# Kernel optimization log

Measured on AMD Instinct MI355X. Metric: run time of the kernel, lower is better.

Reference implementation:

```python
import jax, jax.numpy as jnp
import numpy as np

OBS, SEQ = 8, 12          # observed steps, predicted steps (seq_len init arg)
G, P = 96, 16             # scenes x pedestrians per scene (uniform groups)
B = G * P                 # 1536
H, E, BOT, MID = 128, 64, 1024, 512


def setup_inputs() -> dict:
    key = jax.random.key(0)
    ks = jax.random.split(key, 26)
    rn = lambda k, sh, s=0.05: jax.random.normal(k, sh, jnp.float32) * s
    starts = jnp.arange(G, dtype=jnp.int64) * P
    return {
        "obs_traj": rn(ks[0], (OBS, B, 2), 1.0),
        "obs_traj_rel": rn(ks[1], (OBS, B, 2), 1.0),
        "typeID_seq": rn(ks[2], (OBS, B, 1), 1.0),
        "h0": rn(ks[3], (1, B, H), 0.1),
        "c0": rn(ks[4], (1, B, H), 0.1),
        "seq_start_end": jnp.stack([starts, starts + P], axis=1),
        # decoder spatial embedding Linear(2, E)
        "W_emb": rn(ks[5], (E, 2)), "b_emb": rn(ks[6], (E,)),
        # LSTM(E, H) weights, gate order i,f,g,o (PyTorch convention)
        "W_ih": rn(ks[7], (4 * H, E)), "b_ih": rn(ks[8], (4 * H,)),
        "W_hh": rn(ks[9], (4 * H, H)), "b_hh": rn(ks[10], (4 * H,)),
        # hidden2pos Linear(H, 2)
        "W_pos": rn(ks[11], (2, H)), "b_pos": rn(ks[12], (2,)),
        # PoolHiddenNet: spatial_embedding Linear(2, E), mlp_pre_pool [E+H, 512, BOT]
        "Wp_emb": rn(ks[13], (E, 2)), "bp_emb": rn(ks[14], (E,)),
        "Wp1": rn(ks[15], (MID, E + H)), "bp1": rn(ks[16], (MID,)),
        "Wp2": rn(ks[17], (BOT, MID)), "bp2": rn(ks[18], (BOT,)),
        # Decoder mlp [H+BOT, mlp_dim, H]
        "Wm1": rn(ks[19], (1024, H + BOT)), "bm1": rn(ks[20], (1024,)),
        "Wm2": rn(ks[21], (H, 1024)), "bm2": rn(ks[22], (H,)),
    }


def _forward(obs_traj, obs_traj_rel, h0, c0,
             W_emb, b_emb, W_ih, b_ih, W_hh, b_hh, W_pos, b_pos,
             Wp_emb, bp_emb, Wp1, bp1, Wp2, bp2, Wm1, bm1, Wm2, bm2):
    batch = obs_traj.shape[1]

    def pool(h, pos):
        # uniform groups: h_states.view(-1,H)[start:end] == reshape to (G,P,H)
        hh = h.reshape(G, P, H)
        pp = pos.reshape(G, P, 2)
        # torch semantics: row (i,j) holds pos[j]-pos[i] and hidden[j]
        rel = pp[:, None, :, :] - pp[:, :, None, :]          # (G,Pi,Pj,2)
        emb = rel @ Wp_emb.T + bp_emb                        # (G,Pi,Pj,E)
        hb = jnp.broadcast_to(hh[:, None, :, :], (G, P, P, H))
        x = jnp.concatenate([emb, hb], axis=-1)              # (G,Pi,Pj,E+H)
        x = jax.nn.relu(x @ Wp1.T + bp1)
        x = jax.nn.relu(x @ Wp2.T + bp2)                     # (G,Pi,Pj,BOT)
        return x.max(axis=2).reshape(batch, BOT)             # max over neighbors j

    def step(carry, _):
        h, c, last_pos, dec_in = carry
        gates = dec_in @ W_ih.T + b_ih + h @ W_hh.T + b_hh
        i, f, g, o = jnp.split(gates, 4, axis=-1)
        c = jax.nn.sigmoid(f) * c + jax.nn.sigmoid(i) * jnp.tanh(g)
        h = jax.nn.sigmoid(o) * jnp.tanh(c)
        rel_pos = h @ W_pos.T + b_pos                        # (B,2)
        curr_pos = rel_pos + last_pos
        pool_h = pool(h, curr_pos)
        ctx = jnp.concatenate([h, pool_h], axis=-1)          # (B,H+BOT)
        h = jax.nn.relu(jax.nn.relu(ctx @ Wm1.T + bm1) @ Wm2.T + bm2)
        dec_in = rel_pos @ W_emb.T + b_emb
        return (h, c, curr_pos, dec_in), rel_pos

    dec_in0 = obs_traj_rel[-1] @ W_emb.T + b_emb
    carry0 = (h0[0], c0[0], obs_traj[-1], dec_in0)
    (h, c, _, _), rels = jax.lax.scan(step, carry0, None, length=SEQ)
    return rels, h[None]                                     # (SEQ,B,2), (1,B,H)


def reference(obs_traj, obs_traj_rel, typeID_seq, h0, c0, seq_start_end,
              W_emb, b_emb, W_ih, b_ih, W_hh, b_hh, W_pos, b_pos,
              Wp_emb, bp_emb, Wp1, bp1, Wp2, bp2, Wm1, bm1, Wm2, bm2):
    # typeID_seq / seq_start_end unused math-wise (typeID module off; groups uniform)
    return _forward(obs_traj, obs_traj_rel, h0, c0,
                    W_emb, b_emb, W_ih, b_ih, W_hh, b_hh, W_pos, b_pos,
                    Wp_emb, bp_emb, Wp1, bp1, Wp2, bp2, Wm1, bm1, Wm2, bm2)
```

## Files before the change

### kernel.cpp

```cpp
#include <hip/hip_runtime.h>
#include <math.h>

#define OBS 8
#define SEQL 12
#define G 96
#define PP 16
#define B 1536
#define HD 128
#define ED 64
#define BOT 1024
#define MIDD 512
#define CTXD (HD + BOT)
#define MLPH 1024

typedef __attribute__((ext_vector_type(8))) short bf16x8;
typedef __attribute__((ext_vector_type(4))) float f32x4;

__device__ inline short f2bf(float x) {
    union { float f; unsigned u; } v; v.f = x;
    unsigned r = v.u + 0x7fffu + ((v.u >> 16) & 1u);
    return (short)(r >> 16);
}

__global__ void swizzleB_kernel(const float* __restrict__ src, unsigned short* __restrict__ dst,
                                int NT, int K, int total) {
    int u = blockIdx.x * 256 + threadIdx.x;
    if (u >= total) return;
    int l = u & 63; int v = u >> 6; int nt = v % NT; int kt = v / NT;
    int n = nt * 16 + (l & 15);
    int k = kt * 32 + ((l >> 4) << 3);
    const float* s = src + n * K + k;
    float4 s0 = *(const float4*)s;
    float4 s1 = *(const float4*)(s + 4);
    bf16x8 o;
    o[0] = f2bf(s0.x); o[1] = f2bf(s0.y); o[2] = f2bf(s0.z); o[3] = f2bf(s0.w);
    o[4] = f2bf(s1.x); o[5] = f2bf(s1.y); o[6] = f2bf(s1.z); o[7] = f2bf(s1.w);
    *(bf16x8*)(dst + u * 8) = o;
}

__global__ void swizzle_cat_kernel(const float* __restrict__ W_ih, const float* __restrict__ W_hh,
                                   unsigned short* __restrict__ dst) {
    int u = blockIdx.x * 256 + threadIdx.x;
    if (u >= 6 * 32 * 64) return;
    int l = u & 63; int v = u >> 6; int nt = v & 31; int kt = v >> 5;
    int n = nt * 16 + (l & 15);
    int k0 = kt * 32 + ((l >> 4) << 3);
    bf16x8 o;
#pragma unroll
    for (int e = 0; e < 8; ++e) {
        int k = k0 + e;
        float val = (k < ED) ? W_ih[n * ED + k] : W_hh[n * HD + (k - ED)];
        o[e] = f2bf(val);
    }
    *(bf16x8*)(dst + u * 8) = o;
}

__global__ void swizzle_p1_kernel(const float* __restrict__ Wp1,
                                  const float* __restrict__ CV,
                                  unsigned short* __restrict__ dst) {
    int u = blockIdx.x * 256 + threadIdx.x;
    if (u >= 5 * 32 * 64) return;
    int l = u & 63; int v = u >> 6; int nt = v & 31; int kt = v >> 5;
    int n = nt * 16 + (l & 15);
    int k0 = kt * 32 + ((l >> 4) << 3);
    bf16x8 o;
#pragma unroll
    for (int e = 0; e < 8; ++e) {
        int k = k0 + e;
        float val;
        if (k < HD)           val = Wp1[n * (ED + HD) + ED + k];
        else if (k == HD + 2) val = CV[n];
        else                  val = 0.f;
        o[e] = f2bf(val);
    }
    *(bf16x8*)(dst + u * 8) = o;
}

__global__ void mcvec_kernel(const float* __restrict__ Wp1, const float* __restrict__ Wp_emb,
                             const float* __restrict__ bp_emb, const float* __restrict__ bp1,
                             float* __restrict__ M0, float* __restrict__ M1, float* __restrict__ CV) {
    int r = blockIdx.x * blockDim.x + threadIdx.x;
    if (r >= MIDD) return;
    float m0 = 0.f, m1 = 0.f, cv = 0.f;
    for (int e = 0; e < ED; ++e) {
        float w = Wp1[r * (ED + HD) + e];
        m0 += w * Wp_emb[e * 2 + 0];
        m1 += w * Wp_emb[e * 2 + 1];
        cv += w * bp_emb[e];
    }
    M0[r] = m0; M1[r] = m1; CV[r] = cv + bp1[r];
}

__global__ void m01f_kernel(const float* __restrict__ M0, const float* __restrict__ M1,
                            float* __restrict__ M0F, float* __restrict__ M1F) {
    int id = blockIdx.x * 256 + threadIdx.x;
    if (id >= 16 * 64 * 8) return;
    int e = id & 7;
    int lane = (id >> 3) & 63;
    int kt = id >> 9;
    int k = kt * 32 + ((lane >> 4) << 3) + e;
    M0F[id] = M0[k];
    M1F[id] = M1[k];
}

__global__ void init_kernel(const float* __restrict__ obs_traj, const float* __restrict__ obs_traj_rel,
                            const float* __restrict__ h0, const float* __restrict__ c0,
                            const float* __restrict__ W_emb, const float* __restrict__ b_emb,
                            float* __restrict__ Hb, float* __restrict__ Cb,
                            float* __restrict__ POSb, float* __restrict__ DIN) {
    int b = blockIdx.x;
    int t = threadIdx.x;
    Hb[b * HD + t] = h0[b * HD + t];
    Cb[b * HD + t] = c0[b * HD + t];
    if (t < 2) POSb[b * 2 + t] = obs_traj[((OBS - 1) * B + b) * 2 + t];
    if (t < ED) {
        float rx = obs_traj_rel[((OBS - 1) * B + b) * 2 + 0];
        float ry = obs_traj_rel[((OBS - 1) * B + b) * 2 + 1];
        DIN[b * ED + t] = W_emb[t * 2 + 0] * rx + W_emb[t * 2 + 1] * ry + b_emb[t];
    }
}

__global__ __launch_bounds__(512) void step_kernel(
    const unsigned short* __restrict__ WcatF, const float* __restrict__ b_ih,
    const float* __restrict__ b_hh,
    const float* __restrict__ W_pos, const float* __restrict__ b_pos,
    const float* __restrict__ W_emb, const float* __restrict__ b_emb,
    const unsigned short* __restrict__ Wp1F2,
    float* __restrict__ Hb, float* __restrict__ Cb, float* __restrict__ POSb,
    float* __restrict__ DIN, unsigned short* __restrict__ Hbf,
    float* __restrict__ AbF, float* __restrict__ rel_out) {

    __shared__ unsigned short gf[6 * 64 * 8];
    __shared__ unsigned short a2f[5 * 64 * 8];
    __shared__ float hsh[16 * HD];
    __shared__ float relsh[16][4];

    int gsc = blockIdx.x;
    int t = threadIdx.x;
    int lane = t & 63, w = t >> 6;
    int colid = lane & 15, quad = lane >> 4;

    if (t < 384) {
        int kt = t >> 6;
        int j = lane & 15;
        int b = gsc * PP + j;
        int k0 = kt * 32 + ((lane >> 4) << 3);
        float4 x0, x1;
        if (k0 < ED) {
            const float4* p = (const float4*)(DIN + b * ED + k0);
            x0 = p[0]; x1 = p[1];
        } else {
            const float4* p = (const float4*)(Hb + b * HD + (k0 - ED));
            x0 = p[0]; x1 = p[1];
        }
        bf16x8 o;
        o[0] = f2bf(x0.x); o[1] = f2bf(x0.y); o[2] = f2bf(x0.z); o[3] = f2bf(x0.w);
        o[4] = f2bf(x1.x); o[5] = f2bf(x1.y); o[6] = f2bf(x1.z); o[7] = f2bf(x1.w);
        *(bf16x8*)(gf + t * 8) = o;
    }
    __syncthreads();

    f32x4 acc[4];
#pragma unroll
    for (int gi = 0; gi < 4; ++gi) acc[gi] = (f32x4)0.f;
#pragma unroll
    for (int kt = 0; kt < 6; ++kt) {
        bf16x8 af = *(const bf16x8*)(gf + (kt * 64 + lane) * 8);
#pragma unroll
        for (int gi = 0; gi < 4; ++gi) {
            bf16x8 bfr = *(const bf16x8*)(WcatF + ((kt * 32 + gi * 8 + w) * 64 + lane) * 8);
            acc[gi] = __builtin_amdgcn_mfma_f32_16x16x32_bf16(af, bfr, acc[gi], 0, 0, 0);
        }
    }
    int hcol = w * 16 + colid;
    float bias[4];
#pragma unroll
    for (int gi = 0; gi < 4; ++gi) {
        int n = (gi * 8 + w) * 16 + colid;
        bias[gi] = b_ih[n] + b_hh[n];
    }
#pragma unroll
    for (int r = 0; r < 4; ++r) {
        int row = quad * 4 + r;
        int b = gsc * PP + row;
        float gI = acc[0][r] + bias[0];
        float gF = acc[1][r] + bias[1];
        float gG = acc[2][r] + bias[2];
        float gO = acc[3][r] + bias[3];
        float c = Cb[b * HD + hcol];
        float cn = (1.f / (1.f + expf(-gF))) * c + (1.f / (1.f + expf(-gI))) * tanhf(gG);
        float hn = (1.f / (1.f + expf(-gO))) * tanhf(cn);
        Cb[b * HD + hcol] = cn;
        Hbf[b * HD + hcol] = (unsigned short)f2bf(hn);
        hsh[row * HD + hcol] = hn;
    }
    __syncthreads();

    {
        int row = t >> 5, kk = t & 31;
        float r0 = 0.f, r1 = 0.f;
#pragma unroll
        for (int q = 0; q < 4; ++q) {
            int k = kk + q * 32;
            float hv = hsh[row * HD + k];
            r0 = fmaf(hv, W_pos[k], r0);
            r1 = fmaf(hv, W_pos[HD + k], r1);
        }
#pragma unroll
        for (int m = 16; m >= 1; m >>= 1) {
            r0 += __shfl_xor(r0, m, 64);
            r1 += __shfl_xor(r1, m, 64);
        }
        if (kk == 0) {
            int b = gsc * PP + row;
            r0 += b_pos[0]; r1 += b_pos[1];
            float px = POSb[b * 2 + 0] + r0;
            float py = POSb[b * 2 + 1] + r1;
            POSb[b * 2 + 0] = px; POSb[b * 2 + 1] = py;
            rel_out[b * 2 + 0] = r0; rel_out[b * 2 + 1] = r1;
            relsh[row][0] = r0; relsh[row][1] = r1; relsh[row][2] = px; relsh[row][3] = py;
        }
    }
    __syncthreads();

#pragma unroll
    for (int rep = 0; rep < 2; ++rep) {
        int idx = rep * 512 + t;
        int row = idx >> 6, e = idx & 63;
        int b = gsc * PP + row;
        DIN[b * ED + e] = W_emb[e * 2 + 0] * relsh[row][0] +
                          W_emb[e * 2 + 1] * relsh[row][1] + b_emb[e];
    }
    if (t < 320) {
        int kt = t >> 6;
        int j = lane & 15;
        int k0 = kt * 32 + ((lane >> 4) << 3);
        bf16x8 o;
#pragma unroll
        for (int e = 0; e < 8; ++e) {
            int k = k0 + e;
            float v;
            if (k < HD)            v = hsh[j * HD + k];
            else if (k == HD + 2)  v = 1.f;
            else                   v = 0.f;
            o[e] = f2bf(v);
        }
        *(bf16x8*)(a2f + t * 8) = o;
    }
    __syncthreads();

    f32x4 acc2[4];
#pragma unroll
    for (int q = 0; q < 4; ++q) acc2[q] = (f32x4)0.f;
#pragma unroll
    for (int kt = 0; kt < 5; ++kt) {
        bf16x8 af = *(const bf16x8*)(a2f + (kt * 64 + lane) * 8);
#pragma unroll
        for (int q = 0; q < 4; ++q) {
            bf16x8 bfr = *(const bf16x8*)(Wp1F2 + ((kt * 32 + w * 4 + q) * 64 + lane) * 8);
            acc2[q] = __builtin_amdgcn_mfma_f32_16x16x32_bf16(af, bfr, acc2[q], 0, 0, 0);
        }
    }
#pragma unroll
    for (int q = 0; q < 4; ++q)
#pragma unroll
        for (int r = 0; r < 4; ++r) {
            int j = quad * 4 + r;
            int k = (w * 4 + q) * 16 + colid;
            int kt2 = k >> 5, lk = (k >> 3) & 3, e = k & 7;
            AbF[((gsc * 16 + kt2) * 64 + lk * 16 + j) * 8 + e] = acc2[q][r];
        }
}

__global__ __launch_bounds__(256, 3) void pool_gemm9_kernel(
    const float* __restrict__ AbF, const float* __restrict__ POSb,
    const float* __restrict__ M0F, const float* __restrict__ M1F,
    const unsigned short* __restrict__ Wp2F, const float* __restrict__ bp2,
    unsigned short* __restrict__ POOLbf) {

    __shared__ __align__(16) unsigned short Bst[2][8 * 64 * 8];
    __shared__ __align__(16) float Ust[2][64 * 8];
    __shared__ __align__(16) float M0st[2][64 * 8];
    __shared__ __align__(16) float M1st[2][64 * 8];

    int bi = blockIdx.x;
    int g = bi % 96;
    int rest = bi / 96;
    int io = rest >> 3;
    int colq = rest & 7;
    int t = threadIdx.x, lane = t & 63, w = t >> 6;
    int i0 = io * 8 + w * 2;
    int j = lane & 15;
    int ntb = colq * 8;

    float pjx = POSb[(g * PP + j) * 2 + 0];
    float pjy = POSb[(g * PP + j) * 2 + 1];
    float dx[2], dy[2];
#pragma unroll
    for (int p = 0; p < 2; ++p) {
        int gi = g * PP + i0 + p;
        dx[p] = pjx - POSb[gi * 2 + 0];
        dy[p] = pjy - POSb[gi * 2 + 1];
    }

    const float* ag = AbF + (size_t)g * (16 * 64 * 8);

    auto stage = [&](int kt, int buf) {
#pragma unroll
        for (int r = 0; r < 2; ++r) {
            int u = r * 256 + t;
            int nt = u >> 6, l = u & 63;
            *(bf16x8*)&Bst[buf][u * 8] =
                *(const bf16x8*)(Wp2F + ((kt * 64 + ntb + nt) * 64 + l) * 8);
        }
        if (t < 128) {
            *(float4*)&Ust[buf][t * 4] = *(const float4*)(ag + kt * 512 + t * 4);
            *(float4*)&M1st[buf][t * 4] = *(const float4*)(M1F + kt * 512 + t * 4);
        } else {
            int q = t - 128;
            *(float4*)&M0st[buf][q * 4] = *(const float4*)(M0F + kt * 512 + q * 4);
        }
    };

    f32x4 acc[2][8];
#pragma unroll
    for (int p = 0; p < 2; ++p)
#pragma unroll
        for (int n = 0; n < 8; ++n) acc[p][n] = (f32x4)0.f;

    stage(0, 0);
    __syncthreads();

    for (int kt = 0; kt < 16; ++kt) {
        int buf = kt & 1;
        if (kt < 15) stage(kt + 1, buf ^ 1);

        const float4* up = (const float4*)&Ust[buf][lane * 8];
        float4 u0 = up[0], u1 = up[1];
        const float4* m0p = (const float4*)&M0st[buf][lane * 8];
        float4 m00 = m0p[0], m01 = m0p[1];
        const float4* m1p = (const float4*)&M1st[buf][lane * 8];
        float4 m10 = m1p[0], m11 = m1p[1];

        bf16x8 af[2];
#pragma unroll
        for (int p = 0; p < 2; ++p) {
            float dxp = dx[p], dyp = dy[p];
            af[p][0] = f2bf(fmaxf(fmaf(m10.x, dyp, fmaf(m00.x, dxp, u0.x)), 0.f));
            af[p][1] = f2bf(fmaxf(fmaf(m10.y, dyp, fmaf(m00.y, dxp, u0.y)), 0.f));
            af[p][2] = f2bf(fmaxf(fmaf(m10.z, dyp, fmaf(m00.z, dxp, u0.z)), 0.f));
            af[p][3] = f2bf(fmaxf(fmaf(m10.w, dyp, fmaf(m00.w, dxp, u0.w)), 0.f));
            af[p][4] = f2bf(fmaxf(fmaf(m11.x, dyp, fmaf(m01.x, dxp, u1.x)), 0.f));
            af[p][5] = f2bf(fmaxf(fmaf(m11.y, dyp, fmaf(m01.y, dxp, u1.y)), 0.f));
            af[p][6] = f2bf(fmaxf(fmaf(m11.z, dyp, fmaf(m01.z, dxp, u1.z)), 0.f));
            af[p][7] = f2bf(fmaxf(fmaf(m11.w, dyp, fmaf(m01.w, dxp, u1.w)), 0.f));
        }
#pragma unroll
        for (int ng = 0; ng < 2; ++ng) {
            bf16x8 bfr[4];
#pragma unroll
            for (int n = 0; n < 4; ++n)
                bfr[n] = *(const bf16x8*)&Bst[buf][((ng * 4 + n) * 64 + lane) * 8];
#pragma unroll
            for (int n = 0; n < 4; ++n) {
                acc[0][ng * 4 + n] =
                    __builtin_amdgcn_mfma_f32_16x16x32_bf16(af[0], bfr[n], acc[0][ng * 4 + n], 0, 0, 0);
                acc[1][ng * 4 + n] =
                    __builtin_amdgcn_mfma_f32_16x16x32_bf16(af[1], bfr[n], acc[1][ng * 4 + n], 0, 0, 0);
            }
        }
        __syncthreads();
    }

    int quad = lane >> 4, colid = lane & 15;
#pragma unroll
    for (int p = 0; p < 2; ++p) {
        int i = g * PP + i0 + p;
#pragma unroll
        for (int n = 0; n < 8; ++n) {
            float m = fmaxf(fmaxf(acc[p][n][0], acc[p][n][1]),
                            fmaxf(acc[p][n][2], acc[p][n][3]));
            m = fmaxf(m, __shfl_xor(m, 16, 64));
            m = fmaxf(m, __shfl_xor(m, 32, 64));
            if (quad == 0) {
                int col = (ntb + n) * 16 + colid;
                float v = fmaxf(m + bp2[col], 0.f);
                POOLbf[i * BOT + col] = (unsigned short)f2bf(v);
            }
        }
    }
}

__global__ __launch_bounds__(256) void mlp1_mfma_kernel(
    const unsigned short* __restrict__ Hbf, const unsigned short* __restrict__ POOLbf,
    const unsigned short* __restrict__ Wm1F, const float* __restrict__ bm1,
    unsigned short* __restrict__ Y1Mbf) {

    __shared__ unsigned short a_f[16 * 64 * 8];
    int mg = blockIdx.x;
    int ng = blockIdx.y;
    int t = threadIdx.x, lane = t & 63, w = t >> 6;
    int rh = w >> 1, nh = w & 1;

    f32x4 acc[2][2];
#pragma unroll
    for (int a = 0; a < 2; ++a)
#pragma unroll
        for (int b = 0; b < 2; ++b) acc[a][b] = (f32x4)0.f;

    for (int c = 0; c < 9; ++c) {
        __syncthreads();
#pragma unroll
        for (int u0 = 0; u0 < 1024; u0 += 256) {
            int u = u0 + t;
            int rg = u >> 8, kt = (u >> 6) & 3, l = u & 63;
            int row = mg * 64 + rg * 16 + (l & 15);
            int kl = kt * 32 + ((l >> 4) << 3);
            const unsigned short* src = (c == 0) ? (Hbf + row * HD + kl)
                                                 : (POOLbf + row * BOT + (c - 1) * 128 + kl);
            *(bf16x8*)(a_f + u * 8) = *(const bf16x8*)src;
        }
        __syncthreads();
#pragma unroll
        for (int kt = 0; kt < 4; ++kt) {
            int ktg = c * 4 + kt;
            bf16x8 bfr[2];
#pragma unroll
            for (int j = 0; j < 2; ++j) {
                int ntg = ng * 4 + nh * 2 + j;
                bfr[j] = *(const bf16x8*)(Wm1F + ((ktg * 64 + ntg) * 64 + lane) * 8);
            }
#pragma unroll
            for (int ri = 0; ri < 2; ++ri) {
                int rg = rh * 2 + ri;
                bf16x8 af = *(const bf16x8*)(a_f + ((rg * 4 + kt) * 64 + lane) * 8);
#pragma unroll
                for (int j = 0; j < 2; ++j)
                    acc[ri][j] = __builtin_amdgcn_mfma_f32_16x16x32_bf16(af, bfr[j], acc[ri][j], 0, 0, 0);
            }
        }
    }
    int quad = lane >> 4, colid = lane & 15;
#pragma unroll
    for (int ri = 0; ri < 2; ++ri)
#pragma unroll
        for (int j = 0; j < 2; ++j) {
            int col = ng * 64 + (nh * 2 + j) * 16 + colid;
            float bb = bm1[col];
#pragma unroll
            for (int r = 0; r < 4; ++r) {
                int row = mg * 64 + (rh * 2 + ri) * 16 + quad * 4 + r;
                float v = fmaxf(acc[ri][j][r] + bb, 0.f);
                Y1Mbf[row * MLPH + col] = (unsigned short)f2bf(v);
            }
        }
}

__global__ __launch_bounds__(256) void mlp2_mfma_kernel(
    const unsigned short* __restrict__ Y1Mbf, const unsigned short* __restrict__ Wm2F,
    const float* __restrict__ bm2, float* __restrict__ Hb, float* __restrict__ hout) {

    __shared__ unsigned short a_f[32 * 64 * 8];
    int rg = blockIdx.x;
    int t = threadIdx.x, lane = t & 63, w = t >> 6;

#pragma unroll
    for (int u0 = 0; u0 < 2048; u0 += 256) {
        int u = u0 + t;
        int kt = u >> 6, l = u & 63;
        int row = rg * 16 + (l & 15);
        int kl = kt * 32 + ((l >> 4) << 3);
        *(bf16x8*)(a_f + u * 8) = *(const bf16x8*)(Y1Mbf + row * MLPH + kl);
    }
    __syncthreads();

    f32x4 acc[2];
    acc[0] = (f32x4)0.f; acc[1] = (f32x4)0.f;
    for (int kt = 0; kt < 32; ++kt) {
        bf16x8 af = *(const bf16x8*)(a_f + (kt * 64 + lane) * 8);
#pragma unroll
        for (int j = 0; j < 2; ++j) {
            int ntg = w * 2 + j;
            bf16x8 bfr = *(const bf16x8*)(Wm2F + ((kt * 8 + ntg) * 64 + lane) * 8);
            acc[j] = __builtin_amdgcn_mfma_f32_16x16x32_bf16(af, bfr, acc[j], 0, 0, 0);
        }
    }
    int quad = lane >> 4, colid = lane & 15;
#pragma unroll
    for (int j = 0; j < 2; ++j) {
        int col = (w * 2 + j) * 16 + colid;
        float bb = bm2[col];
#pragma unroll
        for (int r = 0; r < 4; ++r) {
            int row = rg * 16 + quad * 4 + r;
            float v = fmaxf(acc[j][r] + bb, 0.f);
            Hb[row * HD + col] = v;
            if (hout) hout[row * HD + col] = v;
        }
    }
}

extern "C" void kernel_launch(void* const* d_in, const int* in_sizes, int n_in,
                              void* d_out, int out_size, void* d_ws, size_t ws_size,
                              hipStream_t stream) {
    const float* obs_traj     = (const float*)d_in[0];
    const float* obs_traj_rel = (const float*)d_in[1];
    const float* h0    = (const float*)d_in[3];
    const float* c0    = (const float*)d_in[4];
    const float* W_emb = (const float*)d_in[6];
    const float* b_emb = (const float*)d_in[7];
    const float* W_ih  = (const float*)d_in[8];
    const float* b_ih  = (const float*)d_in[9];
    const float* W_hh  = (const float*)d_in[10];
    const float* b_hh  = (const float*)d_in[11];
    const float* W_pos = (const float*)d_in[12];
    const float* b_pos = (const float*)d_in[13];
    const float* Wp_emb= (const float*)d_in[14];
    const float* bp_emb= (const float*)d_in[15];
    const float* Wp1   = (const float*)d_in[16];
    const float* bp1   = (const float*)d_in[17];
    const float* Wp2   = (const float*)d_in[18];
    const float* bp2   = (const float*)d_in[19];
    const float* Wm1   = (const float*)d_in[20];
    const float* bm1   = (const float*)d_in[21];
    const float* Wm2   = (const float*)d_in[22];
    const float* bm2   = (const float*)d_in[23];

    float* ws = (float*)d_ws;
    float* Hb    = ws; ws += B * HD;
    float* Cb    = ws; ws += B * HD;
    float* POSb  = ws; ws += B * 2;
    float* DIN   = ws; ws += B * ED;
    float* AbF   = ws; ws += B * MIDD;
    float* M0    = ws; ws += MIDD;
    float* M1    = ws; ws += MIDD;
    float* CV    = ws; ws += MIDD;
    float* M0F   = ws; ws += 16 * 64 * 8;
    float* M1F   = ws; ws += 16 * 64 * 8;
    unsigned short* us = (unsigned short*)ws;
    unsigned short* Hbf    = us; us += B * HD;
    unsigned short* POOLbf = us; us += B * BOT;
    unsigned short* Y1Mbf  = us; us += B * MLPH;
    unsigned short* WcatF  = us; us += 6 * 32 * 64 * 8;
    unsigned short* Wp1F2  = us; us += 5 * 32 * 64 * 8;
    unsigned short* Wp2F   = us; us += MIDD * BOT;
    unsigned short* Wm1F   = us; us += CTXD * MLPH;
    unsigned short* Wm2F   = us; us += MLPH * HD;

    float* out = (float*)d_out;
    float* rels_out = out;
    float* h_out    = out + SEQL * B * 2;

    {
        int tot = 16 * 64 * 64;
        swizzleB_kernel<<<(tot + 255) / 256, 256, 0, stream>>>(Wp2, Wp2F, 64, MIDD, tot);
        tot = 36 * 64 * 64;
        swizzleB_kernel<<<(tot + 255) / 256, 256, 0, stream>>>(Wm1, Wm1F, 64, CTXD, tot);
        tot = 32 * 8 * 64;
        swizzleB_kernel<<<(tot + 255) / 256, 256, 0, stream>>>(Wm2, Wm2F, 8, MLPH, tot);
        swizzle_cat_kernel<<<(6 * 32 * 64 + 255) / 256, 256, 0, stream>>>(W_ih, W_hh, WcatF);
    }
    mcvec_kernel<<<2, 256, 0, stream>>>(Wp1, Wp_emb, bp_emb, bp1, M0, M1, CV);
    swizzle_p1_kernel<<<(5 * 32 * 64 + 255) / 256, 256, 0, stream>>>(Wp1, CV, Wp1F2);
    m01f_kernel<<<32, 256, 0, stream>>>(M0, M1, M0F, M1F);
    init_kernel<<<B, 128, 0, stream>>>(obs_traj, obs_traj_rel, h0, c0, W_emb, b_emb,
                                       Hb, Cb, POSb, DIN);

    for (int s = 0; s < SEQL; ++s) {
        step_kernel<<<G, 512, 0, stream>>>(
            WcatF, b_ih, b_hh, W_pos, b_pos, W_emb, b_emb, Wp1F2,
            Hb, Cb, POSb, DIN, Hbf, AbF, rels_out + s * B * 2);
        pool_gemm9_kernel<<<G * 16, 256, 0, stream>>>(AbF, POSb, M0F, M1F, Wp2F, bp2, POOLbf);
        mlp1_mfma_kernel<<<dim3(24, 16), 256, 0, stream>>>(Hbf, POOLbf, Wm1F, bm1, Y1Mbf);
        mlp2_mfma_kernel<<<G, 256, 0, stream>>>(Y1Mbf, Wm2F, bm2, Hb,
                                                (s == SEQL - 1) ? h_out : (float*)nullptr);
    }
}
```

Before: 1.083 ms.

## Widen pool GEMM tile to 256 columns and repack U/M staging in LDS

The pooling GEMM kernel now computes 16 column tiles per block instead of 8, halving the grid to G*8 blocks, so each block's computed A fragments (relu of U + M0*dx + M1*dy) are reused across twice as many MFMAs. The U, M0 and M1 staging buffers are merged into one array with a lane-contiguous float4 layout, so every thread issues a load instead of splitting by thread range. The cost is doubled accumulator registers (32 f32x4 per thread), launch bounds lowered to 2 waves per SIMD, fewer blocks, and a larger shared-memory footprint per block.

```diff
diff --git a/kernel.cpp b/kernel.cpp
--- a/kernel.cpp
+++ b/kernel.cpp
@@ -272,26 +272,24 @@
         }
 }
 
-__global__ __launch_bounds__(256, 3) void pool_gemm9_kernel(
+__global__ __launch_bounds__(256, 2) void pool_gemm10_kernel(
     const float* __restrict__ AbF, const float* __restrict__ POSb,
     const float* __restrict__ M0F, const float* __restrict__ M1F,
     const unsigned short* __restrict__ Wp2F, const float* __restrict__ bp2,
     unsigned short* __restrict__ POOLbf) {
 
-    __shared__ __align__(16) unsigned short Bst[2][8 * 64 * 8];
-    __shared__ __align__(16) float Ust[2][64 * 8];
-    __shared__ __align__(16) float M0st[2][64 * 8];
-    __shared__ __align__(16) float M1st[2][64 * 8];
+    __shared__ __align__(16) unsigned short Bst[2][16 * 64 * 8];
+    __shared__ __align__(16) float UMst[2][6][64 * 4];
 
     int bi = blockIdx.x;
     int g = bi % 96;
     int rest = bi / 96;
-    int io = rest >> 3;
-    int colq = rest & 7;
+    int io = rest >> 2;
+    int colq = rest & 3;
     int t = threadIdx.x, lane = t & 63, w = t >> 6;
     int i0 = io * 8 + w * 2;
     int j = lane & 15;
-    int ntb = colq * 8;
+    int ntb = colq * 16;
 
     float pjx = POSb[(g * PP + j) * 2 + 0];
     float pjy = POSb[(g * PP + j) * 2 + 1];
@@ -307,26 +305,31 @@
 
     auto stage = [&](int kt, int buf) {
 #pragma unroll
-        for (int r = 0; r < 2; ++r) {
+        for (int r = 0; r < 4; ++r) {
             int u = r * 256 + t;
             int nt = u >> 6, l = u & 63;
             *(bf16x8*)&Bst[buf][u * 8] =
                 *(const bf16x8*)(Wp2F + ((kt * 64 + ntb + nt) * 64 + l) * 8);
         }
-        if (t < 128) {
-            *(float4*)&Ust[buf][t * 4] = *(const float4*)(ag + kt * 512 + t * 4);
-            *(float4*)&M1st[buf][t * 4] = *(const float4*)(M1F + kt * 512 + t * 4);
-        } else {
-            int q = t - 128;
-            *(float4*)&M0st[buf][q * 4] = *(const float4*)(M0F + kt * 512 + q * 4);
+        {
+            int pt = t >> 6;
+            int l = t & 63;
+            const float* src = (pt < 2) ? (ag + kt * 512 + l * 8 + pt * 4)
+                                        : (M0F + kt * 512 + l * 8 + (pt - 2) * 4);
+            *(float4*)&UMst[buf][pt][l * 4] = *(const float4*)src;
+            if (t < 128) {
+                int pt2 = 4 + (t >> 6);
+                *(float4*)&UMst[buf][pt2][l * 4] =
+                    *(const float4*)(M1F + kt * 512 + l * 8 + (t >> 6) * 4);
+            }
         }
     };
 
-    f32x4 acc[2][8];
+    f32x4 acc[2][16];
 #pragma unroll
     for (int p = 0; p < 2; ++p)
 #pragma unroll
-        for (int n = 0; n < 8; ++n) acc[p][n] = (f32x4)0.f;
+        for (int n = 0; n < 16; ++n) acc[p][n] = (f32x4)0.f;
 
     stage(0, 0);
     __syncthreads();
@@ -335,12 +338,12 @@
         int buf = kt & 1;
         if (kt < 15) stage(kt + 1, buf ^ 1);
 
-        const float4* up = (const float4*)&Ust[buf][lane * 8];
-        float4 u0 = up[0], u1 = up[1];
-        const float4* m0p = (const float4*)&M0st[buf][lane * 8];
-        float4 m00 = m0p[0], m01 = m0p[1];
-        const float4* m1p = (const float4*)&M1st[buf][lane * 8];
-        float4 m10 = m1p[0], m11 = m1p[1];
+        float4 u0  = *(const float4*)&UMst[buf][0][lane * 4];
+        float4 u1  = *(const float4*)&UMst[buf][1][lane * 4];
+        float4 m00 = *(const float4*)&UMst[buf][2][lane * 4];
+        float4 m01 = *(const float4*)&UMst[buf][3][lane * 4];
+        float4 m10 = *(const float4*)&UMst[buf][4][lane * 4];
+        float4 m11 = *(const float4*)&UMst[buf][5][lane * 4];
 
         bf16x8 af[2];
 #pragma unroll
@@ -356,7 +359,7 @@
             af[p][7] = f2bf(fmaxf(fmaf(m11.w, dyp, fmaf(m01.w, dxp, u1.w)), 0.f));
         }
 #pragma unroll
-        for (int ng = 0; ng < 2; ++ng) {
+        for (int ng = 0; ng < 4; ++ng) {
             bf16x8 bfr[4];
 #pragma unroll
             for (int n = 0; n < 4; ++n)
@@ -377,7 +380,7 @@
     for (int p = 0; p < 2; ++p) {
         int i = g * PP + i0 + p;
 #pragma unroll
-        for (int n = 0; n < 8; ++n) {
+        for (int n = 0; n < 16; ++n) {
             float m = fmaxf(fmaxf(acc[p][n][0], acc[p][n][1]),
                             fmaxf(acc[p][n][2], acc[p][n][3]));
             m = fmaxf(m, __shfl_xor(m, 16, 64));
@@ -570,7 +573,7 @@
         step_kernel<<<G, 512, 0, stream>>>(
             WcatF, b_ih, b_hh, W_pos, b_pos, W_emb, b_emb, Wp1F2,
             Hb, Cb, POSb, DIN, Hbf, AbF, rels_out + s * B * 2);
-        pool_gemm9_kernel<<<G * 16, 256, 0, stream>>>(AbF, POSb, M0F, M1F, Wp2F, bp2, POOLbf);
+        pool_gemm10_kernel<<<G * 8, 256, 0, stream>>>(AbF, POSb, M0F, M1F, Wp2F, bp2, POOLbf);
         mlp1_mfma_kernel<<<dim3(24, 16), 256, 0, stream>>>(Hbf, POOLbf, Wm1F, bm1, Y1Mbf);
         mlp2_mfma_kernel<<<G, 256, 0, stream>>>(Y1Mbf, Wm2F, bm2, Hb,
                                                 (s == SEQL - 1) ? h_out : (float*)nullptr);
```

Measured after the change: 1.336 ms. 1.23x slower.
